# Kernel tuning notes

Measured on AMD Instinct MI355X. Metric: run time of the kernel, lower is better.

## Reference

```python
import jax, jax.numpy as jnp
import numpy as np

N, R, C_IN, C_OUT, MODES = 8, 256, 64, 64, 16


def setup_inputs() -> dict:
    key = jax.random.key(0)
    k1, k2, k3, k4, k5 = jax.random.split(key, 5)
    # xavier-like scale used in the torch init: gain/(in*out)*sqrt(in+out) folded into std
    std = (1.0 / (C_IN * C_OUT)) * np.sqrt(2.0)  # small, keeps spectra sane
    return {
        "X": jax.random.normal(k1, (N, R, R, C_IN), dtype=jnp.float32),
        "W_res": jax.random.normal(k2, (C_IN, C_OUT), dtype=jnp.float32) / np.sqrt(C_IN),
        "b_res": jax.random.normal(k3, (C_OUT,), dtype=jnp.float32) * 0.01,
        "fw0": jax.random.normal(k4, (C_IN, C_OUT, MODES, MODES, 2), dtype=jnp.float32) * std,
        "fw1": jax.random.normal(k5, (C_IN, C_OUT, MODES, MODES, 2), dtype=jnp.float32) * std,
    }


def reference(X, W_res, b_res, fw0, fw1):
    # X: [N, r, r, in_dim]
    n, r, _, _ = X.shape
    modes = fw0.shape[2]
    out_dim = fw0.shape[1]

    res = X @ W_res + b_res  # [N, r, r, out_dim]  (dropout p=0.0 -> identity)

    Xc = jnp.transpose(X, (0, 3, 1, 2))  # [N, in, r, r]
    X_ft = jnp.fft.rfft2(Xc, s=(r, r), norm="ortho")  # [N, in, r, r//2+1] complex

    w0 = fw0[..., 0] + 1j * fw0[..., 1]  # [in, out, m, m] complex
    w1 = fw1[..., 0] + 1j * fw1[..., 1]

    top = jnp.einsum("bixy,ioxy->boxy", X_ft[:, :, :modes, :modes], w0)
    bot = jnp.einsum("bixy,ioxy->boxy", X_ft[:, :, r - modes :, :modes], w1)

    out_ft = jnp.zeros((n, out_dim, r, r // 2 + 1), dtype=X_ft.dtype)
    out_ft = out_ft.at[:, :, :modes, :modes].set(top)
    out_ft = out_ft.at[:, :, r - modes :, :modes].set(bot)

    Xo = jnp.fft.irfft2(out_ft, s=(r, r), norm="ortho")  # [N, out, r, r] real
    Xo = jnp.transpose(Xo, (0, 2, 3, 1))  # [N, r, r, out]
    return jax.nn.silu(Xo + res)
```

## Files before the change

kernel.cpp:

```cpp
#include <hip/hip_runtime.h>
#include <math.h>

#define RDIM 256
#define CIN 64
#define COUT 64
#define MODES 16
#define NB 8

typedef short short8 __attribute__((ext_vector_type(8)));
typedef float f32x4 __attribute__((ext_vector_type(4)));

__device__ __forceinline__ unsigned short f2b(float f) {
    unsigned u = __builtin_bit_cast(unsigned, f);
    unsigned r = (u + 0x7FFFu + ((u >> 16) & 1u)) >> 16;
    return (unsigned short)r;
}

__global__ __launch_bounds__(256) void k_tab(const float* __restrict__ Wres,
                                             unsigned short* __restrict__ Tf2,
                                             unsigned short* __restrict__ T2,
                                             unsigned short* __restrict__ WbT,
                                             unsigned short* __restrict__ Tg,
                                             unsigned short* __restrict__ A2) {
    int e = blockIdx.x * 256 + (int)threadIdx.x;
    if (e < 8192) {
        int kyc = e >> 8, k = e & 255;
        int S = k >> 3, j = k & 7;
        int w = S >> 3, h = (S >> 2) & 1, q = S & 3;
        int y = w * 64 + q + 4 * (h * 8 + j);
        int ky = kyc >> 1;
        int p = (ky * y) & 255;
        float ang = (float)p * (float)(2.0 * M_PI / 256.0);
        float sz, cz;
        sincosf(ang, &sz, &cz);
        Tf2[e] = f2b((kyc & 1) ? -sz : cz);
    } else if (e < 40960) {
        int f = e - 8192;
        int r = f >> 9, k = f & 511;
        int S = k >> 3, j = k & 7;
        int w = S >> 4, bp = (S >> 3) & 1, a = S & 7;
        int d = j >> 1, c = j & 1;
        int x = w * 64 + bp + 8 * a + 2 * d;
        int m = r >> 1, cc = r & 1;
        int kx = (m < 16) ? m : (m + 224);
        int p = (kx * x) & 255;
        float ang = (float)p * (float)(2.0 * M_PI / 256.0);
        float sz, cz;
        sincosf(ang, &sz, &cz);
        float val = (cc == 0) ? (c ? sz : cz) : (c ? cz : -sz);
        T2[f] = f2b(val * (1.0f / 256.0f));
    } else if (e < 45056) {
        int f = e - 40960;
        int o = f >> 6, k = f & 63;
        WbT[o * 64 + k] = f2b(Wres[k * 64 + o]);
    } else if (e < 53248) {
        int f = e - 45056;
        int y = f >> 5, kk = f & 31, ky = kk >> 1;
        int p = (ky * y) & 255;
        float ang = (float)p * (float)(2.0 * M_PI / 256.0);
        float sz, cz;
        sincosf(ang, &sz, &cz);
        Tg[f] = f2b((kk & 1) ? -sz : cz);
    } else {
        int f = e - 53248;
        int comp = f >> 14, g = f & 16383;
        int x = g >> 6, k = g & 63;
        int m = k >> 1, c = k & 1;
        int kx = (m < 16) ? m : (m + 224);
        int p = (kx * x) & 255;
        float ang = (float)p * (float)(2.0 * M_PI / 256.0);
        float sz, cz;
        sincosf(ang, &sz, &cz);
        float val = (comp == 0) ? (c ? -sz : cz) : (c ? cz : sz);
        A2[f] = f2b(val);
    }
}

__global__ __launch_bounds__(256) void k_wt(const float* __restrict__ fw0,
                                            const float* __restrict__ fw1,
                                            unsigned short* __restrict__ WTb) {
    __shared__ float2 Ls[64 * 134];
    int bi = blockIdx.x;
    int arr = bi >> 7;
    int iq = (bi >> 3) & 15;
    int oq = (bi >> 1) & 3;
    int h = bi & 1;
    int i0 = iq * 4, o0 = oq * 16;
    const float4* fw4 = (const float4*)(arr ? fw1 : fw0);
    int t = (int)threadIdx.x;
#pragma unroll
    for (int n = 0; n < 16; n++) {
        int idx = n * 256 + t;
        int io = idx >> 6, fi = idx & 63;
        int i_loc = io >> 4, o_loc = io & 15;
        float4 v = fw4[(size_t)((i0 + i_loc) * 64 + o0 + o_loc) * 128 + h * 64 + fi];
        ((float4*)Ls)[io * 67 + fi] = v;
    }
    __syncthreads();
#pragma unroll
    for (int n = 0; n < 16; n++) {
        int u = n * 256 + t;
        int o_loc = u & 15, ky = (u >> 4) & 15, mm = (u >> 8) & 7, var = u >> 11;
        int qL = mm * 16 + ky;
        short8 hh;
#pragma unroll
        for (int j = 0; j < 8; j++) {
            int i_loc = j >> 1, c = j & 1;
            float2 wv = Ls[(i_loc * 16 + o_loc) * 134 + qL];
            float val = var ? (c ? wv.x : wv.y) : (c ? -wv.y : wv.x);
            hh[j] = (short)f2b(val);
        }
        int m = arr * 16 + h * 8 + mm;
        int o = o0 + o_loc;
        *(short8*)(WTb + (size_t)(m * 16 + ky) * 16384 + var * 8192 + iq * 512 + o * 8) = hh;
    }
}

__global__ __launch_bounds__(256) void k_fwd_y(const float* __restrict__ X,
                                               const unsigned short* __restrict__ Tf,
                                               float2* __restrict__ A,
                                               unsigned short* __restrict__ Xbf) {
    __shared__ short8 Xb[64 * 32];
    int b = blockIdx.x >> 8;
    int x = blockIdx.x & 255;
    int t = (int)threadIdx.x;
    int w = t >> 6;
    int l = t & 63;
    int q = l >> 4;
    int f4 = l & 15;
    int i0 = f4 * 4;

    const float4* X4 = (const float4*)(X + ((size_t)(b * 256 + x)) * 256 * 64);
    unsigned short* Xrow = Xbf + ((size_t)(b * 256 + x)) * 16384;
#pragma unroll
    for (int h = 0; h < 2; h++) {
        float4 v[8];
#pragma unroll
        for (int n = 0; n < 8; n++) {
            int y = w * 64 + q + 4 * (h * 8 + n);
            v[n] = X4[y * 16 + f4];
        }
#pragma unroll
        for (int n = 0; n < 8; n++) {
            int y = w * 64 + q + 4 * (h * 8 + n);
            *(ushort4*)(Xrow + (size_t)y * 64 + i0) =
                make_ushort4(f2b(v[n].x), f2b(v[n].y), f2b(v[n].z), f2b(v[n].w));
        }
        const float* vf = (const float*)v;
        int s = w * 8 + h * 4 + q;
#pragma unroll
        for (int di = 0; di < 4; di++) {
            int i = i0 + di;
            short8 hb;
#pragma unroll
            for (int j = 0; j < 8; j++) hb[j] = (short)f2b(vf[j * 4 + di]);
            Xb[i * 32 + (s ^ (i & 7))] = hb;
        }
    }
    __syncthreads();

    int m16 = l & 15;
    int quad = l >> 4;
    int iRow = w * 16 + m16;
    int isw = iRow & 7;

    f32x4 acc0 = (f32x4){0.f, 0.f, 0.f, 0.f};
    f32x4 acc1 = (f32x4){0.f, 0.f, 0.f, 0.f};
    const unsigned short* T0 = Tf + (size_t)m16 * 256 + quad * 8;
#pragma unroll
    for (int ks = 0; ks < 8; ks++) {
        short8 a0 = *(const short8*)(T0 + ks * 32);
        short8 a1 = *(const short8*)(T0 + 4096 + ks * 32);
        short8 bfrag = Xb[iRow * 32 + ((ks * 4 + quad) ^ isw)];
        acc0 = __builtin_amdgcn_mfma_f32_16x16x32_bf16(a0, bfrag, acc0, 0, 0, 0);
        acc1 = __builtin_amdgcn_mfma_f32_16x16x32_bf16(a1, bfrag, acc1, 0, 0, 0);
    }

    float2* Ab = A + ((size_t)(b * 16) * 256 + x) * 64;
    int ky0 = quad * 2;
    Ab[(size_t)(ky0)     * 16384 + iRow] = make_float2(acc0[0], acc0[1]);
    Ab[(size_t)(ky0 + 1) * 16384 + iRow] = make_float2(acc0[2], acc0[3]);
    Ab[(size_t)(ky0 + 8) * 16384 + iRow] = make_float2(acc1[0], acc1[1]);
    Ab[(size_t)(ky0 + 9) * 16384 + iRow] = make_float2(acc1[2], acc1[3]);
}

__global__ __launch_bounds__(256) void k_fwd_x(const float2* __restrict__ A,
                                               const unsigned short* __restrict__ T2,
                                               float2* __restrict__ C) {
    __shared__ short8 Bs[32 * 64];
    int bi = blockIdx.x;
    int b = bi >> 5;
    int ky = (bi >> 1) & 15;
    int ih = bi & 1;
    int t = (int)threadIdx.x;
    int w = t >> 6, l = t & 63;
    int ip = l & 15;
    int bp = (l >> 4) & 1;
    int ab = l >> 5;
    const float4* A4 = (const float4*)(A + ((size_t)(b * 16 + ky)) * 16384);
#pragma unroll
    for (int aa = 0; aa < 4; aa++) {
        int a = ab * 4 + aa;
        float4 v[4];
#pragma unroll
        for (int d4 = 0; d4 < 4; d4++) {
            int xx = w * 64 + bp + 8 * a + 2 * d4;
            v[d4] = A4[xx * 32 + ih * 16 + ip];
        }
        int S = w * 16 + bp * 8 + a;
        short8 h0, h1;
        h0[0] = (short)f2b(v[0].x); h0[1] = (short)f2b(v[0].y);
        h0[2] = (short)f2b(v[1].x); h0[3] = (short)f2b(v[1].y);
        h0[4] = (short)f2b(v[2].x); h0[5] = (short)f2b(v[2].y);
        h0[6] = (short)f2b(v[3].x); h0[7] = (short)f2b(v[3].y);
        h1[0] = (short)f2b(v[0].z); h1[1] = (short)f2b(v[0].w);
        h1[2] = (short)f2b(v[1].z); h1[3] = (short)f2b(v[1].w);
        h1[4] = (short)f2b(v[2].z); h1[5] = (short)f2b(v[2].w);
        h1[6] = (short)f2b(v[3].z); h1[7] = (short)f2b(v[3].w);
        int iL0 = ip * 2, iL1 = iL0 + 1;
        Bs[iL0 * 64 + (S ^ (iL0 & 7))] = h0;
        Bs[iL1 * 64 + (S ^ (iL1 & 7))] = h1;
    }
    __syncthreads();

    int m16 = l & 15, quad = l >> 4;
    f32x4 acc[2];
    acc[0] = (f32x4){0.f, 0.f, 0.f, 0.f};
    acc[1] = (f32x4){0.f, 0.f, 0.f, 0.f};
    const unsigned short* Tp = T2 + (size_t)(w * 16 + m16) * 512 + quad * 8;
#pragma unroll
    for (int ks = 0; ks < 16; ks++) {
        short8 af = *(const short8*)(Tp + ks * 32);
#pragma unroll
        for (int nt = 0; nt < 2; nt++) {
            int iL = nt * 16 + m16;
            short8 bfr = Bs[iL * 64 + ((ks * 4 + quad) ^ (iL & 7))];
            acc[nt] = __builtin_amdgcn_mfma_f32_16x16x32_bf16(af, bfr, acc[nt], 0, 0, 0);
        }
    }

    float2* Cb = C + ((size_t)(b * 16 + ky)) * 2048;
    int m0 = w * 8 + quad * 2;
#pragma unroll
    for (int nt = 0; nt < 2; nt++) {
        int ig = ih * 32 + nt * 16 + m16;
        Cb[(size_t)m0 * 64 + ig]       = make_float2(acc[nt][0], acc[nt][1]);
        Cb[(size_t)(m0 + 1) * 64 + ig] = make_float2(acc[nt][2], acc[nt][3]);
    }
}

__global__ __launch_bounds__(256) void k_mix(const float2* __restrict__ C,
                                             const unsigned short* __restrict__ WTb,
                                             float2* __restrict__ D) {
    __shared__ float Csf[8 * 132];
    int bi = blockIdx.x;
    int ky = bi >> 5, m = bi & 31;
    int t = (int)threadIdx.x;
    {
        int bq = t >> 5;
        int e = t & 31;
        const float4* src = (const float4*)(C + (((size_t)bq * 16 + ky) * 32 + m) * 64);
        ((float4*)Csf)[bq * 33 + e] = src[e];
    }
    __syncthreads();
    int w = t >> 6, l = t & 63;
    int var = w >> 1, ntb = (w & 1) * 2;
    int m16 = l & 15, quad = l >> 4;
    const unsigned short* Wp = WTb + (size_t)(m * 16 + ky) * 16384 + var * 8192;
    const float* cp0 = Csf + (m16 & 7) * 132 + quad * 8;
    f32x4 acc[2];
    acc[0] = (f32x4){0.f, 0.f, 0.f, 0.f};
    acc[1] = (f32x4){0.f, 0.f, 0.f, 0.f};
#pragma unroll
    for (int ks = 0; ks < 4; ks++) {
        const float* cp = cp0 + ks * 32;
        short8 af;
#pragma unroll
        for (int j = 0; j < 8; j++) af[j] = (short)f2b(cp[j]);
        int oct = ks * 4 + quad;
#pragma unroll
        for (int n2 = 0; n2 < 2; n2++) {
            int o = (ntb + n2) * 16 + m16;
            short8 bfr = *(const short8*)(Wp + oct * 512 + o * 8);
            acc[n2] = __builtin_amdgcn_mfma_f32_16x16x32_bf16(af, bfr, acc[n2], 0, 0, 0);
        }
    }
    if (quad < 2) {
#pragma unroll
        for (int n2 = 0; n2 < 2; n2++) {
            int o = (ntb + n2) * 16 + m16;
#pragma unroll
            for (int r = 0; r < 4; r++) {
                int bb = quad * 4 + r;
                float* dp = (float*)&D[(((size_t)bb * 16 + ky) * 32 + m) * 64 + o];
                dp[var] = acc[n2][r];
            }
        }
    }
}

__global__ __launch_bounds__(256) void k_inv_x(const float2* __restrict__ D,
                                               const unsigned short* __restrict__ A2,
                                               float2* __restrict__ G) {
    __shared__ short8 Bd[64 * 8];
    int bi = blockIdx.x;
    int b = bi >> 5;
    int ky = (bi >> 1) & 15;
    int xh = bi & 1;
    int t = (int)threadIdx.x;
    int w = t >> 6, l = t & 63;
    const float2* Dp = D + ((size_t)(b * 16 + ky)) * 2048;
    float2 dv[8];
#pragma unroll
    for (int s = 0; s < 8; s++) dv[s] = Dp[(size_t)(w * 8 + s) * 64 + l];
    short8 h0, h1;
    h0[0] = (short)f2b(dv[0].x); h0[1] = (short)f2b(dv[0].y);
    h0[2] = (short)f2b(dv[1].x); h0[3] = (short)f2b(dv[1].y);
    h0[4] = (short)f2b(dv[2].x); h0[5] = (short)f2b(dv[2].y);
    h0[6] = (short)f2b(dv[3].x); h0[7] = (short)f2b(dv[3].y);
    h1[0] = (short)f2b(dv[4].x); h1[1] = (short)f2b(dv[4].y);
    h1[2] = (short)f2b(dv[5].x); h1[3] = (short)f2b(dv[5].y);
    h1[4] = (short)f2b(dv[6].x); h1[5] = (short)f2b(dv[6].y);
    h1[6] = (short)f2b(dv[7].x); h1[7] = (short)f2b(dv[7].y);
    int sl = l & 7;
    Bd[l * 8 + ((2 * w) ^ sl)]     = h0;
    Bd[l * 8 + ((2 * w + 1) ^ sl)] = h1;
    __syncthreads();

    int m16 = l & 15, quad = l >> 4;
    int x0 = xh * 128 + w * 32;
    f32x4 acc[2][4][2];
#pragma unroll
    for (int mt = 0; mt < 2; mt++)
#pragma unroll
        for (int nt = 0; nt < 4; nt++)
#pragma unroll
            for (int c = 0; c < 2; c++) acc[mt][nt][c] = (f32x4){0.f, 0.f, 0.f, 0.f};

#pragma unroll
    for (int ks = 0; ks < 2; ks++) {
        short8 ar[2], ai[2];
#pragma unroll
        for (int mt = 0; mt < 2; mt++) {
            int xr = x0 + mt * 16 + m16;
            ar[mt] = *(const short8*)(A2 + (size_t)xr * 64 + ks * 32 + quad * 8);
            ai[mt] = *(const short8*)(A2 + 16384 + (size_t)xr * 64 + ks * 32 + quad * 8);
        }
#pragma unroll
        for (int nt = 0; nt < 4; nt++) {
            int o = nt * 16 + m16;
            short8 bf = Bd[o * 8 + ((ks * 4 + quad) ^ (o & 7))];
#pragma unroll
            for (int mt = 0; mt < 2; mt++) {
                acc[mt][nt][0] = __builtin_amdgcn_mfma_f32_16x16x32_bf16(ar[mt], bf, acc[mt][nt][0], 0, 0, 0);
                acc[mt][nt][1] = __builtin_amdgcn_mfma_f32_16x16x32_bf16(ai[mt], bf, acc[mt][nt][1], 0, 0, 0);
            }
        }
    }

#pragma unroll
    for (int mt = 0; mt < 2; mt++)
#pragma unroll
        for (int nt = 0; nt < 4; nt++) {
            int o = nt * 16 + m16;
#pragma unroll
            for (int r = 0; r < 4; r++) {
                int x = x0 + mt * 16 + quad * 4 + r;
                G[((size_t)(b * 256 + x) * 16 + ky) * 64 + o] =
                    make_float2(acc[mt][nt][0][r], acc[mt][nt][1][r]);
            }
        }
}

__global__ __launch_bounds__(256) void k_out(const unsigned short* __restrict__ Xbf,
                                             const float2* __restrict__ G,
                                             const unsigned short* __restrict__ WbT,
                                             const unsigned short* __restrict__ Tg,
                                             const float* __restrict__ bres,
                                             float* __restrict__ out) {
    __shared__ unsigned short Bsp[64 * 32];
    int b = blockIdx.x >> 8;
    int x = blockIdx.x & 255;
    int t = (int)threadIdx.x;

    const float2* Gp = G + ((size_t)(b * 256 + x)) * 16 * 64;
    for (int e = t; e < 1024; e += 256) {
        int ky = e >> 6, o = e & 63;
        float2 g = Gp[e];
        float sc = (ky == 0) ? (1.0f / 256.0f) : (2.0f / 256.0f);
        Bsp[o * 32 + 2 * ky]     = f2b(g.x * sc);
        Bsp[o * 32 + 2 * ky + 1] = f2b(g.y * sc);
    }
    __syncthreads();

    int w = t >> 6;
    int l = t & 63;
    int m16 = l & 15;
    int quad = l >> 4;

    short8 bw0[4], bw1[4], bs[4];
    float br[4];
#pragma unroll
    for (int nt = 0; nt < 4; nt++) {
        int o = nt * 16 + m16;
        bw0[nt] = *(const short8*)(WbT + o * 64 + quad * 8);
        bw1[nt] = *(const short8*)(WbT + o * 64 + 32 + quad * 8);
        bs[nt]  = *(const short8*)(Bsp + o * 32 + quad * 8);
        br[nt]  = bres[o];
    }

    const unsigned short* Xrow = Xbf + ((size_t)(b * 256 + x)) * 16384;
    float* orow = out + ((size_t)(b * 256 + x)) * 256 * 64;

    f32x4 acc[4][4];
#pragma unroll
    for (int mt = 0; mt < 4; mt++)
#pragma unroll
        for (int nt = 0; nt < 4; nt++) acc[mt][nt] = (f32x4){0.f, 0.f, 0.f, 0.f};

#pragma unroll
    for (int mt = 0; mt < 4; mt++) {
        int y = w * 64 + mt * 16 + m16;
        short8 a0 = *(const short8*)(Xrow + (size_t)y * 64 + quad * 8);
        short8 a1 = *(const short8*)(Xrow + (size_t)y * 64 + 32 + quad * 8);
        short8 aT = *(const short8*)(Tg + (size_t)y * 32 + quad * 8);
#pragma unroll
        for (int nt = 0; nt < 4; nt++) {
            acc[mt][nt] = __builtin_amdgcn_mfma_f32_16x16x32_bf16(a0, bw0[nt], acc[mt][nt], 0, 0, 0);
            acc[mt][nt] = __builtin_amdgcn_mfma_f32_16x16x32_bf16(a1, bw1[nt], acc[mt][nt], 0, 0, 0);
            acc[mt][nt] = __builtin_amdgcn_mfma_f32_16x16x32_bf16(aT, bs[nt],  acc[mt][nt], 0, 0, 0);
        }
    }

#pragma unroll
    for (int mt = 0; mt < 4; mt++) {
#pragma unroll
        for (int nt = 0; nt < 4; nt++) {
            int o = nt * 16 + m16;
#pragma unroll
            for (int r = 0; r < 4; r++) {
                int y = w * 64 + mt * 16 + quad * 4 + r;
                float v = acc[mt][nt][r] + br[nt];
                float sg = __builtin_amdgcn_rcpf(1.0f + __expf(-v));
                orow[(size_t)y * 64 + o] = v * sg;
            }
        }
    }
}

extern "C" void kernel_launch(void* const* d_in, const int* in_sizes, int n_in,
                              void* d_out, int out_size, void* d_ws, size_t ws_size,
                              hipStream_t stream) {
    const float* X    = (const float*)d_in[0];
    const float* Wres = (const float*)d_in[1];
    const float* bres = (const float*)d_in[2];
    const float* fw0  = (const float*)d_in[3];
    const float* fw1  = (const float*)d_in[4];
    float* out = (float*)d_out;

    float2* A = (float2*)d_ws;
    float2* C = A + 2097152;
    float2* D = C + 262144;
    unsigned short* WTb = (unsigned short*)(D + 262144);
    unsigned short* Xbf = WTb + 8388608;
    unsigned short* Tf2 = Xbf + 33554432;
    unsigned short* T2  = Tf2 + 8192;
    unsigned short* WbT = T2 + 32768;
    unsigned short* Tg  = WbT + 4096;
    unsigned short* A2  = Tg + 8192;
    float2* G = A;

    k_tab<<<336, 256, 0, stream>>>(Wres, Tf2, T2, WbT, Tg, A2);
    k_wt<<<256, 256, 0, stream>>>(fw0, fw1, WTb);
    k_fwd_y<<<NB * 256, 256, 0, stream>>>(X, Tf2, A, Xbf);
    k_fwd_x<<<256, 256, 0, stream>>>(A, T2, C);
    k_mix<<<512, 256, 0, stream>>>(C, WTb, D);
    k_inv_x<<<256, 256, 0, stream>>>(D, A2, G);
    k_out<<<NB * 256, 256, 0, stream>>>(Xbf, G, WbT, Tg, bres, out);
}
```

Measured before the change: 310.8 us.

## Fuse forward-x DFT, spectral mixing and inverse-x DFT into one kernel

Merges k_fwd_x, k_mix and k_inv_x into a single k_spec kernel, one 512-thread block per (batch, ky). The x-direction DFT result and the mixed spectrum now stay in shared memory instead of going through global buffers C and D. The spectral mixing switches from bf16 MFMA to scalar fp32 complex FMAs over a float2 weight layout, and the two table-prep kernels are merged into one launch. This removes two launches and two global round trips. The cost is only 128 blocks on the device, scalar mixing math, and a G buffer that no longer aliases A.

```diff
diff --git a/kernel.cpp b/kernel.cpp
--- a/kernel.cpp
+++ b/kernel.cpp
@@ -16,103 +16,91 @@
     return (unsigned short)r;
 }
 
-__global__ __launch_bounds__(256) void k_tab(const float* __restrict__ Wres,
-                                             unsigned short* __restrict__ Tf2,
-                                             unsigned short* __restrict__ T2,
-                                             unsigned short* __restrict__ WbT,
-                                             unsigned short* __restrict__ Tg,
-                                             unsigned short* __restrict__ A2) {
-    int e = blockIdx.x * 256 + (int)threadIdx.x;
-    if (e < 8192) {
-        int kyc = e >> 8, k = e & 255;
-        int S = k >> 3, j = k & 7;
-        int w = S >> 3, h = (S >> 2) & 1, q = S & 3;
-        int y = w * 64 + q + 4 * (h * 8 + j);
-        int ky = kyc >> 1;
-        int p = (ky * y) & 255;
-        float ang = (float)p * (float)(2.0 * M_PI / 256.0);
-        float sz, cz;
-        sincosf(ang, &sz, &cz);
-        Tf2[e] = f2b((kyc & 1) ? -sz : cz);
-    } else if (e < 40960) {
-        int f = e - 8192;
-        int r = f >> 9, k = f & 511;
-        int S = k >> 3, j = k & 7;
-        int w = S >> 4, bp = (S >> 3) & 1, a = S & 7;
-        int d = j >> 1, c = j & 1;
-        int x = w * 64 + bp + 8 * a + 2 * d;
-        int m = r >> 1, cc = r & 1;
-        int kx = (m < 16) ? m : (m + 224);
-        int p = (kx * x) & 255;
-        float ang = (float)p * (float)(2.0 * M_PI / 256.0);
-        float sz, cz;
-        sincosf(ang, &sz, &cz);
-        float val = (cc == 0) ? (c ? sz : cz) : (c ? cz : -sz);
-        T2[f] = f2b(val * (1.0f / 256.0f));
-    } else if (e < 45056) {
-        int f = e - 40960;
-        int o = f >> 6, k = f & 63;
-        WbT[o * 64 + k] = f2b(Wres[k * 64 + o]);
-    } else if (e < 53248) {
-        int f = e - 45056;
-        int y = f >> 5, kk = f & 31, ky = kk >> 1;
-        int p = (ky * y) & 255;
-        float ang = (float)p * (float)(2.0 * M_PI / 256.0);
-        float sz, cz;
-        sincosf(ang, &sz, &cz);
-        Tg[f] = f2b((kk & 1) ? -sz : cz);
+__global__ __launch_bounds__(256) void k_prep(const float* __restrict__ Wres,
+                                              const float* __restrict__ fw0,
+                                              const float* __restrict__ fw1,
+                                              unsigned short* __restrict__ Tf2,
+                                              unsigned short* __restrict__ T2,
+                                              unsigned short* __restrict__ WbT,
+                                              unsigned short* __restrict__ Tg,
+                                              unsigned short* __restrict__ A2,
+                                              float2* __restrict__ WT) {
+    __shared__ float2 Ls[16][257];
+    int bi = blockIdx.x;
+    int t = (int)threadIdx.x;
+    if (bi < 336) {
+        int e = bi * 256 + t;
+        if (e < 8192) {
+            int kyc = e >> 8, k = e & 255;
+            int S = k >> 3, j = k & 7;
+            int w = S >> 3, h = (S >> 2) & 1, q = S & 3;
+            int y = w * 64 + q + 4 * (h * 8 + j);
+            int ky = kyc >> 1;
+            int p = (ky * y) & 255;
+            float ang = (float)p * (float)(2.0 * M_PI / 256.0);
+            float sz, cz;
+            sincosf(ang, &sz, &cz);
+            Tf2[e] = f2b((kyc & 1) ? -sz : cz);
+        } else if (e < 40960) {
+            int f = e - 8192;
+            int r = f >> 9, k = f & 511;
+            int S = k >> 3, j = k & 7;
+            int w = S >> 4, bp = (S >> 3) & 1, a = S & 7;
+            int d = j >> 1, c = j & 1;
+            int x = w * 64 + bp + 8 * a + 2 * d;
+            int m = r >> 1, cc = r & 1;
+            int kx = (m < 16) ? m : (m + 224);
+            int p = (kx * x) & 255;
+            float ang = (float)p * (float)(2.0 * M_PI / 256.0);
+            float sz, cz;
+            sincosf(ang, &sz, &cz);
+            float val = (cc == 0) ? (c ? sz : cz) : (c ? cz : -sz);
+            T2[f] = f2b(val * (1.0f / 256.0f));
+        } else if (e < 45056) {
+            int f = e - 40960;
+            int o = f >> 6, k = f & 63;
+            WbT[o * 64 + k] = f2b(Wres[k * 64 + o]);
+        } else if (e < 53248) {
+            int f = e - 45056;
+            int y = f >> 5, kk = f & 31, ky = kk >> 1;
+            int p = (ky * y) & 255;
+            float ang = (float)p * (float)(2.0 * M_PI / 256.0);
+            float sz, cz;
+            sincosf(ang, &sz, &cz);
+            Tg[f] = f2b((kk & 1) ? -sz : cz);
+        } else {
+            int f = e - 53248;
+            int comp = f >> 14, g = f & 16383;
+            int x = g >> 6, k = g & 63;
+            int m = k >> 1, c = k & 1;
+            int kx = (m < 16) ? m : (m + 224);
+            int p = (kx * x) & 255;
+            float ang = (float)p * (float)(2.0 * M_PI / 256.0);
+            float sz, cz;
+            sincosf(ang, &sz, &cz);
+            float val = (comp == 0) ? (c ? -sz : cz) : (c ? cz : sz);
+            A2[f] = f2b(val);
+        }
     } else {
-        int f = e - 53248;
-        int comp = f >> 14, g = f & 16383;
-        int x = g >> 6, k = g & 63;
-        int m = k >> 1, c = k & 1;
-        int kx = (m < 16) ? m : (m + 224);
-        int p = (kx * x) & 255;
-        float ang = (float)p * (float)(2.0 * M_PI / 256.0);
-        float sz, cz;
-        sincosf(ang, &sz, &cz);
-        float val = (comp == 0) ? (c ? -sz : cz) : (c ? cz : sz);
-        A2[f] = f2b(val);
-    }
-}
-
-__global__ __launch_bounds__(256) void k_wt(const float* __restrict__ fw0,
-                                            const float* __restrict__ fw1,
-                                            unsigned short* __restrict__ WTb) {
-    __shared__ float2 Ls[64 * 134];
-    int bi = blockIdx.x;
-    int arr = bi >> 7;
-    int iq = (bi >> 3) & 15;
-    int oq = (bi >> 1) & 3;
-    int h = bi & 1;
-    int i0 = iq * 4, o0 = oq * 16;
-    const float4* fw4 = (const float4*)(arr ? fw1 : fw0);
-    int t = (int)threadIdx.x;
-#pragma unroll
-    for (int n = 0; n < 16; n++) {
-        int idx = n * 256 + t;
-        int io = idx >> 6, fi = idx & 63;
-        int i_loc = io >> 4, o_loc = io & 15;
-        float4 v = fw4[(size_t)((i0 + i_loc) * 64 + o0 + o_loc) * 128 + h * 64 + fi];
-        ((float4*)Ls)[io * 67 + fi] = v;
-    }
-    __syncthreads();
-#pragma unroll
-    for (int n = 0; n < 16; n++) {
-        int u = n * 256 + t;
-        int o_loc = u & 15, ky = (u >> 4) & 15, mm = (u >> 8) & 7, var = u >> 11;
-        int qL = mm * 16 + ky;
-        short8 hh;
-#pragma unroll
-        for (int j = 0; j < 8; j++) {
-            int i_loc = j >> 1, c = j & 1;
-            float2 wv = Ls[(i_loc * 16 + o_loc) * 134 + qL];
-            float val = var ? (c ? wv.x : wv.y) : (c ? -wv.y : wv.x);
-            hh[j] = (short)f2b(val);
-        }
-        int m = arr * 16 + h * 8 + mm;
-        int o = o0 + o_loc;
-        *(short8*)(WTb + (size_t)(m * 16 + ky) * 16384 + var * 8192 + iq * 512 + o * 8) = hh;
+        int blk = bi - 336;
+        int arr = blk >> 8;
+        int tile = blk & 255;
+        const float2* s2 = (const float2*)(arr ? fw1 : fw0);
+        for (int e = t; e < 4096; e += 256) {
+            int oo = e >> 8;
+            int q = e & 255;
+            Ls[oo][q] = s2[(size_t)(tile * 16 + oo) * 256 + q];
+        }
+        __syncthreads();
+        int i = (tile * 16) >> 6;
+        int o0 = (tile * 16) & 63;
+        for (int e = t; e < 4096; e += 256) {
+            int oo = e & 15;
+            int q = e >> 4;
+            int mx = q >> 4, ky = q & 15;
+            int m = arr * 16 + mx;
+            WT[((size_t)(m * 16 + ky) * 64 + i) * 64 + o0 + oo] = Ls[oo][q];
+        }
     }
 }
 
@@ -184,192 +172,155 @@
     Ab[(size_t)(ky0 + 9) * 16384 + iRow] = make_float2(acc1[2], acc1[3]);
 }
 
-__global__ __launch_bounds__(256) void k_fwd_x(const float2* __restrict__ A,
-                                               const unsigned short* __restrict__ T2,
-                                               float2* __restrict__ C) {
-    __shared__ short8 Bs[32 * 64];
+__global__ __launch_bounds__(512) void k_spec(const float2* __restrict__ A,
+                                              const unsigned short* __restrict__ T2,
+                                              const float2* __restrict__ WT,
+                                              const unsigned short* __restrict__ A2,
+                                              float2* __restrict__ G) {
+    __shared__ char Lsm[65536];
+    short8* Bs = (short8*)Lsm;
+    float2* Cf = (float2*)Lsm;
+    short8* Bd = (short8*)(Lsm + 16384);
+
     int bi = blockIdx.x;
-    int b = bi >> 5;
-    int ky = (bi >> 1) & 15;
-    int ih = bi & 1;
+    int b = bi >> 4;
+    int ky = bi & 15;
     int t = (int)threadIdx.x;
-    int w = t >> 6, l = t & 63;
-    int ip = l & 15;
-    int bp = (l >> 4) & 1;
-    int ab = l >> 5;
-    const float4* A4 = (const float4*)(A + ((size_t)(b * 16 + ky)) * 16384);
-#pragma unroll
-    for (int aa = 0; aa < 4; aa++) {
-        int a = ab * 4 + aa;
-        float4 v[4];
-#pragma unroll
-        for (int d4 = 0; d4 < 4; d4++) {
-            int xx = w * 64 + bp + 8 * a + 2 * d4;
-            v[d4] = A4[xx * 32 + ih * 16 + ip];
-        }
-        int S = w * 16 + bp * 8 + a;
-        short8 h0, h1;
-        h0[0] = (short)f2b(v[0].x); h0[1] = (short)f2b(v[0].y);
-        h0[2] = (short)f2b(v[1].x); h0[3] = (short)f2b(v[1].y);
-        h0[4] = (short)f2b(v[2].x); h0[5] = (short)f2b(v[2].y);
-        h0[6] = (short)f2b(v[3].x); h0[7] = (short)f2b(v[3].y);
-        h1[0] = (short)f2b(v[0].z); h1[1] = (short)f2b(v[0].w);
-        h1[2] = (short)f2b(v[1].z); h1[3] = (short)f2b(v[1].w);
-        h1[4] = (short)f2b(v[2].z); h1[5] = (short)f2b(v[2].w);
-        h1[6] = (short)f2b(v[3].z); h1[7] = (short)f2b(v[3].w);
-        int iL0 = ip * 2, iL1 = iL0 + 1;
-        Bs[iL0 * 64 + (S ^ (iL0 & 7))] = h0;
-        Bs[iL1 * 64 + (S ^ (iL1 & 7))] = h1;
+    int w = t >> 6;
+    int l = t & 63;
+
+    {
+        int wx = w & 3, ih = w >> 2;
+        int ip = l & 15, bp = (l >> 4) & 1, ab = l >> 5;
+        const float4* A4 = (const float4*)(A + ((size_t)(b * 16 + ky)) * 16384);
+#pragma unroll
+        for (int aa = 0; aa < 4; aa++) {
+            int a = ab * 4 + aa;
+            float4 v[4];
+#pragma unroll
+            for (int d4 = 0; d4 < 4; d4++) {
+                int xx = wx * 64 + bp + 8 * a + 2 * d4;
+                v[d4] = A4[xx * 32 + ih * 16 + ip];
+            }
+            int S = wx * 16 + bp * 8 + a;
+            short8 h0, h1;
+            h0[0] = (short)f2b(v[0].x); h0[1] = (short)f2b(v[0].y);
+            h0[2] = (short)f2b(v[1].x); h0[3] = (short)f2b(v[1].y);
+            h0[4] = (short)f2b(v[2].x); h0[5] = (short)f2b(v[2].y);
+            h0[6] = (short)f2b(v[3].x); h0[7] = (short)f2b(v[3].y);
+            h1[0] = (short)f2b(v[0].z); h1[1] = (short)f2b(v[0].w);
+            h1[2] = (short)f2b(v[1].z); h1[3] = (short)f2b(v[1].w);
+            h1[4] = (short)f2b(v[2].z); h1[5] = (short)f2b(v[2].w);
+            h1[6] = (short)f2b(v[3].z); h1[7] = (short)f2b(v[3].w);
+            int iL0 = (ih * 16 + ip) * 2, iL1 = iL0 + 1;
+            Bs[iL0 * 64 + (S ^ (iL0 & 7))] = h0;
+            Bs[iL1 * 64 + (S ^ (iL1 & 7))] = h1;
+        }
     }
     __syncthreads();
 
     int m16 = l & 15, quad = l >> 4;
+    int ws_ = w & 3, nh = w >> 2;
     f32x4 acc[2];
     acc[0] = (f32x4){0.f, 0.f, 0.f, 0.f};
     acc[1] = (f32x4){0.f, 0.f, 0.f, 0.f};
-    const unsigned short* Tp = T2 + (size_t)(w * 16 + m16) * 512 + quad * 8;
-#pragma unroll
-    for (int ks = 0; ks < 16; ks++) {
-        short8 af = *(const short8*)(Tp + ks * 32);
-#pragma unroll
-        for (int nt = 0; nt < 2; nt++) {
-            int iL = nt * 16 + m16;
-            short8 bfr = Bs[iL * 64 + ((ks * 4 + quad) ^ (iL & 7))];
-            acc[nt] = __builtin_amdgcn_mfma_f32_16x16x32_bf16(af, bfr, acc[nt], 0, 0, 0);
-        }
-    }
-
-    float2* Cb = C + ((size_t)(b * 16 + ky)) * 2048;
-    int m0 = w * 8 + quad * 2;
-#pragma unroll
-    for (int nt = 0; nt < 2; nt++) {
-        int ig = ih * 32 + nt * 16 + m16;
-        Cb[(size_t)m0 * 64 + ig]       = make_float2(acc[nt][0], acc[nt][1]);
-        Cb[(size_t)(m0 + 1) * 64 + ig] = make_float2(acc[nt][2], acc[nt][3]);
-    }
-}
-
-__global__ __launch_bounds__(256) void k_mix(const float2* __restrict__ C,
-                                             const unsigned short* __restrict__ WTb,
-                                             float2* __restrict__ D) {
-    __shared__ float Csf[8 * 132];
-    int bi = blockIdx.x;
-    int ky = bi >> 5, m = bi & 31;
-    int t = (int)threadIdx.x;
     {
-        int bq = t >> 5;
-        int e = t & 31;
-        const float4* src = (const float4*)(C + (((size_t)bq * 16 + ky) * 32 + m) * 64);
-        ((float4*)Csf)[bq * 33 + e] = src[e];
-    }
-    __syncthreads();
-    int w = t >> 6, l = t & 63;
-    int var = w >> 1, ntb = (w & 1) * 2;
-    int m16 = l & 15, quad = l >> 4;
-    const unsigned short* Wp = WTb + (size_t)(m * 16 + ky) * 16384 + var * 8192;
-    const float* cp0 = Csf + (m16 & 7) * 132 + quad * 8;
-    f32x4 acc[2];
-    acc[0] = (f32x4){0.f, 0.f, 0.f, 0.f};
-    acc[1] = (f32x4){0.f, 0.f, 0.f, 0.f};
-#pragma unroll
-    for (int ks = 0; ks < 4; ks++) {
-        const float* cp = cp0 + ks * 32;
-        short8 af;
-#pragma unroll
-        for (int j = 0; j < 8; j++) af[j] = (short)f2b(cp[j]);
-        int oct = ks * 4 + quad;
+        const unsigned short* Tp = T2 + (size_t)(ws_ * 16 + m16) * 512 + quad * 8;
+#pragma unroll
+        for (int ks = 0; ks < 16; ks++) {
+            short8 af = *(const short8*)(Tp + ks * 32);
+#pragma unroll
+            for (int n2 = 0; n2 < 2; n2++) {
+                int iL = (nh * 2 + n2) * 16 + m16;
+                short8 bfr = Bs[iL * 64 + ((ks * 4 + quad) ^ (iL & 7))];
+                acc[n2] = __builtin_amdgcn_mfma_f32_16x16x32_bf16(af, bfr, acc[n2], 0, 0, 0);
+            }
+        }
+    }
+    __syncthreads();
+
+    {
+        int m0 = ws_ * 8 + quad * 2;
 #pragma unroll
         for (int n2 = 0; n2 < 2; n2++) {
-            int o = (ntb + n2) * 16 + m16;
-            short8 bfr = *(const short8*)(Wp + oct * 512 + o * 8);
-            acc[n2] = __builtin_amdgcn_mfma_f32_16x16x32_bf16(af, bfr, acc[n2], 0, 0, 0);
-        }
-    }
-    if (quad < 2) {
-#pragma unroll
-        for (int n2 = 0; n2 < 2; n2++) {
-            int o = (ntb + n2) * 16 + m16;
-#pragma unroll
-            for (int r = 0; r < 4; r++) {
-                int bb = quad * 4 + r;
-                float* dp = (float*)&D[(((size_t)bb * 16 + ky) * 32 + m) * 64 + o];
-                dp[var] = acc[n2][r];
-            }
-        }
-    }
-}
-
-__global__ __launch_bounds__(256) void k_inv_x(const float2* __restrict__ D,
-                                               const unsigned short* __restrict__ A2,
-                                               float2* __restrict__ G) {
-    __shared__ short8 Bd[64 * 8];
-    int bi = blockIdx.x;
-    int b = bi >> 5;
-    int ky = (bi >> 1) & 15;
-    int xh = bi & 1;
-    int t = (int)threadIdx.x;
-    int w = t >> 6, l = t & 63;
-    const float2* Dp = D + ((size_t)(b * 16 + ky)) * 2048;
-    float2 dv[8];
-#pragma unroll
-    for (int s = 0; s < 8; s++) dv[s] = Dp[(size_t)(w * 8 + s) * 64 + l];
-    short8 h0, h1;
-    h0[0] = (short)f2b(dv[0].x); h0[1] = (short)f2b(dv[0].y);
-    h0[2] = (short)f2b(dv[1].x); h0[3] = (short)f2b(dv[1].y);
-    h0[4] = (short)f2b(dv[2].x); h0[5] = (short)f2b(dv[2].y);
-    h0[6] = (short)f2b(dv[3].x); h0[7] = (short)f2b(dv[3].y);
-    h1[0] = (short)f2b(dv[4].x); h1[1] = (short)f2b(dv[4].y);
-    h1[2] = (short)f2b(dv[5].x); h1[3] = (short)f2b(dv[5].y);
-    h1[4] = (short)f2b(dv[6].x); h1[5] = (short)f2b(dv[6].y);
-    h1[6] = (short)f2b(dv[7].x); h1[7] = (short)f2b(dv[7].y);
-    int sl = l & 7;
-    Bd[l * 8 + ((2 * w) ^ sl)]     = h0;
-    Bd[l * 8 + ((2 * w + 1) ^ sl)] = h1;
-    __syncthreads();
-
-    int m16 = l & 15, quad = l >> 4;
-    int x0 = xh * 128 + w * 32;
-    f32x4 acc[2][4][2];
-#pragma unroll
-    for (int mt = 0; mt < 2; mt++)
-#pragma unroll
-        for (int nt = 0; nt < 4; nt++)
-#pragma unroll
-            for (int c = 0; c < 2; c++) acc[mt][nt][c] = (f32x4){0.f, 0.f, 0.f, 0.f};
-
-#pragma unroll
-    for (int ks = 0; ks < 2; ks++) {
-        short8 ar[2], ai[2];
-#pragma unroll
-        for (int mt = 0; mt < 2; mt++) {
-            int xr = x0 + mt * 16 + m16;
-            ar[mt] = *(const short8*)(A2 + (size_t)xr * 64 + ks * 32 + quad * 8);
-            ai[mt] = *(const short8*)(A2 + 16384 + (size_t)xr * 64 + ks * 32 + quad * 8);
-        }
-#pragma unroll
-        for (int nt = 0; nt < 4; nt++) {
-            int o = nt * 16 + m16;
-            short8 bf = Bd[o * 8 + ((ks * 4 + quad) ^ (o & 7))];
+            int i = (nh * 2 + n2) * 16 + m16;
+            Cf[(size_t)m0 * 64 + i]       = make_float2(acc[0 + n2][0], acc[n2][1]);
+            Cf[(size_t)(m0 + 1) * 64 + i] = make_float2(acc[n2][2], acc[n2][3]);
+        }
+    }
+    __syncthreads();
+
+    {
+        int o = t & 63, mg = t >> 6;
+        float dr[4], di[4];
+#pragma unroll
+        for (int s = 0; s < 4; s++) {
+            int m = mg * 4 + s;
+            const float2* Wp = WT + (size_t)(m * 16 + ky) * 4096 + o;
+            const float2* Cp = Cf + (size_t)m * 64;
+            float drv = 0.f, div = 0.f;
+#pragma unroll 16
+            for (int i = 0; i < 64; i++) {
+                float2 wv = Wp[(size_t)i * 64];
+                float2 cv = Cp[i];
+                drv += cv.x * wv.x - cv.y * wv.y;
+                div += cv.x * wv.y + cv.y * wv.x;
+            }
+            dr[s] = drv; di[s] = div;
+        }
+        short8 h;
+        h[0] = (short)f2b(dr[0]); h[1] = (short)f2b(di[0]);
+        h[2] = (short)f2b(dr[1]); h[3] = (short)f2b(di[1]);
+        h[4] = (short)f2b(dr[2]); h[5] = (short)f2b(di[2]);
+        h[6] = (short)f2b(dr[3]); h[7] = (short)f2b(di[3]);
+        Bd[o * 8 + (mg ^ (o & 7))] = h;
+    }
+    __syncthreads();
+
+    {
+        int x0 = w * 32;
+        f32x4 acc2[2][4][2];
+#pragma unroll
+        for (int mt = 0; mt < 2; mt++)
+#pragma unroll
+            for (int nt = 0; nt < 4; nt++)
+#pragma unroll
+                for (int c = 0; c < 2; c++) acc2[mt][nt][c] = (f32x4){0.f, 0.f, 0.f, 0.f};
+
+#pragma unroll
+        for (int ks = 0; ks < 2; ks++) {
+            short8 ar[2], ai[2];
 #pragma unroll
             for (int mt = 0; mt < 2; mt++) {
-                acc[mt][nt][0] = __builtin_amdgcn_mfma_f32_16x16x32_bf16(ar[mt], bf, acc[mt][nt][0], 0, 0, 0);
-                acc[mt][nt][1] = __builtin_amdgcn_mfma_f32_16x16x32_bf16(ai[mt], bf, acc[mt][nt][1], 0, 0, 0);
-            }
-        }
-    }
-
-#pragma unroll
-    for (int mt = 0; mt < 2; mt++)
-#pragma unroll
-        for (int nt = 0; nt < 4; nt++) {
-            int o = nt * 16 + m16;
-#pragma unroll
-            for (int r = 0; r < 4; r++) {
-                int x = x0 + mt * 16 + quad * 4 + r;
-                G[((size_t)(b * 256 + x) * 16 + ky) * 64 + o] =
-                    make_float2(acc[mt][nt][0][r], acc[mt][nt][1][r]);
-            }
-        }
+                int xr = x0 + mt * 16 + m16;
+                ar[mt] = *(const short8*)(A2 + (size_t)xr * 64 + ks * 32 + quad * 8);
+                ai[mt] = *(const short8*)(A2 + 16384 + (size_t)xr * 64 + ks * 32 + quad * 8);
+            }
+#pragma unroll
+            for (int nt = 0; nt < 4; nt++) {
+                int o2 = nt * 16 + m16;
+                short8 bf = Bd[o2 * 8 + ((ks * 4 + quad) ^ (o2 & 7))];
+#pragma unroll
+                for (int mt = 0; mt < 2; mt++) {
+                    acc2[mt][nt][0] = __builtin_amdgcn_mfma_f32_16x16x32_bf16(ar[mt], bf, acc2[mt][nt][0], 0, 0, 0);
+                    acc2[mt][nt][1] = __builtin_amdgcn_mfma_f32_16x16x32_bf16(ai[mt], bf, acc2[mt][nt][1], 0, 0, 0);
+                }
+            }
+        }
+
+#pragma unroll
+        for (int mt = 0; mt < 2; mt++)
+#pragma unroll
+            for (int nt = 0; nt < 4; nt++) {
+                int o2 = nt * 16 + m16;
+#pragma unroll
+                for (int r = 0; r < 4; r++) {
+                    int x = x0 + mt * 16 + quad * 4 + r;
+                    G[((size_t)(b * 256 + x) * 16 + ky) * 64 + o2] =
+                        make_float2(acc2[mt][nt][0][r], acc2[mt][nt][1][r]);
+                }
+            }
+    }
 }
 
 __global__ __launch_bounds__(256) void k_out(const unsigned short* __restrict__ Xbf,
@@ -458,23 +409,18 @@
     const float* fw1  = (const float*)d_in[4];
     float* out = (float*)d_out;
 
-    float2* A = (float2*)d_ws;
-    float2* C = A + 2097152;
-    float2* D = C + 262144;
-    unsigned short* WTb = (unsigned short*)(D + 262144);
-    unsigned short* Xbf = WTb + 8388608;
+    float2* A  = (float2*)d_ws;
+    float2* G  = A + 2097152;
+    float2* WT = G + 2097152;
+    unsigned short* Xbf = (unsigned short*)(WT + 2097152);
     unsigned short* Tf2 = Xbf + 33554432;
     unsigned short* T2  = Tf2 + 8192;
     unsigned short* WbT = T2 + 32768;
     unsigned short* Tg  = WbT + 4096;
     unsigned short* A2  = Tg + 8192;
-    float2* G = A;
-
-    k_tab<<<336, 256, 0, stream>>>(Wres, Tf2, T2, WbT, Tg, A2);
-    k_wt<<<256, 256, 0, stream>>>(fw0, fw1, WTb);
+
+    k_prep<<<848, 256, 0, stream>>>(Wres, fw0, fw1, Tf2, T2, WbT, Tg, A2, WT);
     k_fwd_y<<<NB * 256, 256, 0, stream>>>(X, Tf2, A, Xbf);
-    k_fwd_x<<<256, 256, 0, stream>>>(A, T2, C);
-    k_mix<<<512, 256, 0, stream>>>(C, WTb, D);
-    k_inv_x<<<256, 256, 0, stream>>>(D, A2, G);
+    k_spec<<<NB * 16, 512, 0, stream>>>(A, T2, WT, A2, G);
     k_out<<<NB * 256, 256, 0, stream>>>(Xbf, G, WbT, Tg, bres, out);
 }
```

Result: no change. 316.8 us (+1.9%).
